# Kernel optimization log

Measured on AMD Instinct MI355X. Metric: run time of the kernel, lower is better.

Reference implementation:

```python
import jax, jax.numpy as jnp
import numpy as np

LEAKY = 0.2  # tf.nn.leaky_relu default alpha
E_SZ = [64, 64, 16]
F_SZ = [128, 128, 8]
N_MAPS, C, H, W = 64, 1, 32, 32
B = 8192


def _leaky(x):
    return jnp.where(x >= 0, x, LEAKY * x)


def func_theta(x, theta, sz, in_sz):
    # x: [B, in_sz]; theta: [B, total]; per-sample MLP with weights sliced from theta
    y = x
    offset = 0
    n = len(sz)
    for i, out_sz in enumerate(sz):
        w_sz = in_sz * out_sz
        Wm = theta[:, offset:offset + w_sz].reshape(-1, in_sz, out_sz)
        offset += w_sz
        b = theta[:, offset:offset + out_sz]
        offset += out_sz
        y = jnp.einsum('bi,bio->bo', y, Wm) + b
        if i < n - 1:
            y = _leaky(y)
        in_sz = out_sz
    return y


def setup_inputs() -> dict:
    key = jax.random.key(0)
    ks = jax.random.split(key, 16)

    def g(k, shape, scale):
        return (jax.random.normal(k, shape, dtype=jnp.float32) * scale)

    inp = {
        'indices': jax.random.randint(ks[0], (B,), 0, N_MAPS, dtype=jnp.int32),
        'states': jax.random.normal(ks[1], (B, 4), dtype=jnp.float32),
        'maps': jax.random.normal(ks[2], (N_MAPS, C, H, W), dtype=jnp.float32),
        'fc1_w': g(ks[3], (C * H * W, 256), 1.0 / np.sqrt(C * H * W)),
        'fc1_b': jnp.zeros((256,), jnp.float32),
        'fc2_w': g(ks[4], (256, 128), 1.0 / np.sqrt(256)),
        'fc2_b': jnp.zeros((128,), jnp.float32),
        'fc3_w': g(ks[5], (128, 128), 1.0 / np.sqrt(128)),
        'fc3_b': jnp.zeros((128,), jnp.float32),
        'bn_w': g(ks[6], (128, 32), 1.0 / np.sqrt(128)),
        'bn_b': jnp.zeros((32,), jnp.float32),
        'e_w': g(ks[7], (32, 5456), 1e-5),
        'e_b': g(ks[8], (5456,), 1e-3),
        'f_w': g(ks[9], (32, 21768), 1e-5),
        'f_b': g(ks[10], (21768,), 1e-3),
    }
    return inp


def reference(indices, states, maps, fc1_w, fc1_b, fc2_w, fc2_b, fc3_w, fc3_b,
              bn_w, bn_b, e_w, e_b, f_w, f_b):
    # gather maps per sample and flatten (NCHW -> NHWC transpose is a no-op after flatten
    # mathematically, but keep the exact data layout of the original)
    m = jnp.transpose(maps[indices], (0, 2, 3, 1)).astype(jnp.float32)  # [B,H,W,C]
    z = m.reshape(m.shape[0], -1)

    # hypernet trunk
    z = _leaky(z @ fc1_w + fc1_b)
    z = _leaky(z @ fc2_w + fc2_b)
    z = _leaky(z @ fc3_w + fc3_b)
    z = z @ bn_w + bn_b  # bottleneck, no activation
    theta_e = z @ e_w + e_b  # [B, 5456]
    theta_f = z @ f_w + f_b  # [B, 21768]

    S = states[:, 0:2]
    G = states[:, 2:4]
    e_s = func_theta(S, theta_e, E_SZ, 2)
    e_g = func_theta(G, theta_e, E_SZ, 2)
    zf = jnp.concatenate([e_s, e_g], axis=-1)  # [B, 32]
    ang = func_theta(zf, theta_f, F_SZ, 2 * E_SZ[-1])  # [B, 8]
    pts = jnp.concatenate([jnp.sin(ang), jnp.cos(ang)], axis=-1)  # [B, 16]
    return pts
```

## Files before the change

### kernel.cpp

```cpp
#include <hip/hip_runtime.h>
#include <hip/hip_bf16.h>


#define LEAKY 0.2f
#define NCLS 64
#define B_TOT 8192
#define NSLICE 4


__device__ __forceinline__ float lrelu(float x) { return x >= 0.f ? x : LEAKY * x; }

__global__ __launch_bounds__(1024) void backbone_bucket_kernel(
    const float* __restrict__ maps,
    const float* __restrict__ fc1_w, const float* __restrict__ fc1_b,
    const float* __restrict__ fc2_w, const float* __restrict__ fc2_b,
    const float* __restrict__ fc3_w, const float* __restrict__ fc3_b,
    const float* __restrict__ bn_w,  const float* __restrict__ bn_b,
    float* __restrict__ z,
    const int* __restrict__ idx, int* __restrict__ counts,
    int* __restrict__ offsets, int* __restrict__ perm)
{
    __shared__ float m[1024];
    __shared__ float red[1024];
    __shared__ float h1[256];
    __shared__ float h2[128];
    __shared__ float h3[128];
    __shared__ int cnt[16][64];
    __shared__ int wcur[16][64];

    const int t = threadIdx.x;

    if (blockIdx.x == 64) {
        const int w = t >> 6;
        cnt[w][t & 63] = 0;
        __syncthreads();
        int my[8];
#pragma unroll
        for (int r = 0; r < 8; ++r) {
            my[r] = idx[r * 1024 + t];
            atomicAdd(&cnt[w][my[r]], 1);
        }
        __syncthreads();
        if (t < 64) {
            int run = 0;
#pragma unroll
            for (int w2 = 0; w2 < 16; ++w2) {
                const int v = cnt[w2][t];
                wcur[w2][t] = run;
                run += v;
            }
            counts[t] = run;
            int x = run;
            for (int d = 1; d < 64; d <<= 1) {
                const int y = __shfl_up(x, d, 64);
                if (t >= d) x += y;
            }
            const int basec = x - run;
            offsets[t] = basec;
#pragma unroll
            for (int w2 = 0; w2 < 16; ++w2) wcur[w2][t] += basec;
        }
        __syncthreads();
#pragma unroll
        for (int r = 0; r < 8; ++r) {
            const int p = atomicAdd(&wcur[w][my[r]], 1);
            perm[p] = r * 1024 + t;
        }
        return;
    }

    const int c = blockIdx.x;
    m[t] = maps[(size_t)c * 1024 + t];
    __syncthreads();

    {
        const int o = t & 255, ks = t >> 8;
        const float* wp = fc1_w + o;
        float acc = 0.f;
#pragma unroll 8
        for (int i = 0; i < 256; ++i) {
            const int k = ks * 256 + i;
            acc += m[k] * wp[(size_t)k * 256];
        }
        red[t] = acc;
    }
    __syncthreads();
    if (t < 256)
        h1[t] = lrelu(fc1_b[t] + red[t] + red[256 + t] + red[512 + t] + red[768 + t]);
    __syncthreads();
    {
        const int o = t & 127, ks = t >> 7;
        float acc = 0.f;
#pragma unroll
        for (int i = 0; i < 32; ++i) {
            const int k = ks * 32 + i;
            acc += h1[k] * fc2_w[k * 128 + o];
        }
        red[t] = acc;
    }
    __syncthreads();
    if (t < 128) {
        float a = fc2_b[t];
#pragma unroll
        for (int r = 0; r < 8; ++r) a += red[r * 128 + t];
        h2[t] = lrelu(a);
    }
    __syncthreads();
    {
        const int o = t & 127, ks = t >> 7;
        float acc = 0.f;
#pragma unroll
        for (int i = 0; i < 16; ++i) {
            const int k = ks * 16 + i;
            acc += h2[k] * fc3_w[k * 128 + o];
        }
        red[t] = acc;
    }
    __syncthreads();
    if (t < 128) {
        float a = fc3_b[t];
#pragma unroll
        for (int r = 0; r < 8; ++r) a += red[r * 128 + t];
        h3[t] = lrelu(a);
    }
    __syncthreads();
    {
        const int o = t & 31, ks = t >> 5;
        float acc = 0.f;
#pragma unroll
        for (int i = 0; i < 4; ++i) {
            const int k = ks * 4 + i;
            acc += h3[k] * bn_w[k * 32 + o];
        }
        red[t] = acc;
    }
    __syncthreads();
    if (t < 32) {
        float a = bn_b[t];
#pragma unroll
        for (int r = 0; r < 32; ++r) a += red[r * 32 + t];
        z[c * 32 + t] = a;
    }
}

__global__ __launch_bounds__(256) void theta_kernel(
    const float* __restrict__ z,
    const float* __restrict__ e_w, const float* __restrict__ e_b,
    const float* __restrict__ f_w, const float* __restrict__ f_b,
    float* __restrict__ th_e, float* __restrict__ th_f)
{
    __shared__ __align__(16) float zl[2048];
    const int t = threadIdx.x;
    ((float4*)zl)[t]       = ((const float4*)z)[t];
    ((float4*)zl)[t + 256] = ((const float4*)z)[t + 256];
    __syncthreads();

    int j = blockIdx.x * 256 + t;
    const int cbase = blockIdx.y * 8;
    const float* wbase;
    float* op;
    int stride;
    float bias;
    if (j < 5456) {
        wbase = e_w + j; bias = e_b[j]; op = th_e + j; stride = 5456;
    } else {
        const int jj = j - 5456;
        if (jj >= 21768) return;
        wbase = f_w + jj; bias = f_b[jj]; op = th_f + jj; stride = 21768;
    }
    float wk[32];
#pragma unroll
    for (int k = 0; k < 32; ++k) wk[k] = wbase[(size_t)k * stride];

#pragma unroll
    for (int cc = 0; cc < 8; cc += 4) {
        const int c0 = cbase + cc;
        float a0 = bias, a1 = bias, a2 = bias, a3 = bias;
#pragma unroll
        for (int k4 = 0; k4 < 8; ++k4) {
            const float4 z0 = *(const float4*)&zl[(c0 + 0) * 32 + k4 * 4];
            const float4 z1 = *(const float4*)&zl[(c0 + 1) * 32 + k4 * 4];
            const float4 z2 = *(const float4*)&zl[(c0 + 2) * 32 + k4 * 4];
            const float4 z3 = *(const float4*)&zl[(c0 + 3) * 32 + k4 * 4];
            const float w0 = wk[k4 * 4], w1 = wk[k4 * 4 + 1];
            const float w2 = wk[k4 * 4 + 2], w3 = wk[k4 * 4 + 3];
            a0 += z0.x * w0 + z0.y * w1 + z0.z * w2 + z0.w * w3;
            a1 += z1.x * w0 + z1.y * w1 + z1.z * w2 + z1.w * w3;
            a2 += z2.x * w0 + z2.y * w1 + z2.z * w2 + z2.w * w3;
            a3 += z3.x * w0 + z3.y * w1 + z3.z * w2 + z3.w * w3;
        }
        op[(size_t)(c0 + 0) * stride] = a0;
        op[(size_t)(c0 + 1) * stride] = a1;
        op[(size_t)(c0 + 2) * stride] = a2;
        op[(size_t)(c0 + 3) * stride] = a3;
    }
}

#define ESTRIDE 68
#define FSTRIDE 132

__global__ __launch_bounds__(512) void func_kernel(
    const float* __restrict__ states,
    const float* __restrict__ th_e_all, const float* __restrict__ th_f_all,
    const int* __restrict__ counts, const int* __restrict__ offsets,
    const int* __restrict__ perm, float* __restrict__ out)
{
    __shared__ __align__(16) float wbuf[5392];
    __shared__ __align__(16) float w3fb[1160];
    __shared__ __align__(16) float actA[4352];
    __shared__ __align__(16) float actB[4352];

    const int c = blockIdx.x;
    const int s = blockIdx.y;
    const int nb   = counts[c];
    const int base = offsets[c];
    const int chunk = (nb + NSLICE - 1) / NSLICE;
    const int k0 = s * chunk;
    const int k1 = (nb < k0 + chunk) ? nb : (k0 + chunk);
    const int cnt = (k1 > k0) ? (k1 - k0) : 0;
    if (cnt == 0) return;

    const float* te = th_e_all + (size_t)c * 5456;
    const float* tf = th_f_all + (size_t)c * 21768;

    const int t  = threadIdx.x;
    const int b  = t & 31;
    const int ve = (t >> 5) & 1;
    const int vb = t & 63;
    const int ge = t >> 6;
    const int gf = t >> 5;
    const int cole = ge * 8;
    const int colf = gf * 8;
    const int eoff = vb * ESTRIDE;
    const int foff = b * FSTRIDE;

    for (int j = t * 4; j < 1160; j += 2048)
        *(float4*)&w3fb[j] = *(const float4*)&tf[20608 + j];
    for (int j = t * 4; j < 5392; j += 2048)
        *(float4*)&wbuf[j] = *(const float4*)&te[j];

    const int passes = (cnt + 31) >> 5;
    for (int p = 0; p < passes; ++p) {
        __syncthreads();
        if (p) {
            for (int j = t * 4; j < 5392; j += 2048)
                *(float4*)&wbuf[j] = *(const float4*)&te[j];
            __syncthreads();
        }

        const int kk = k0 + p * 32 + b;
        const bool valid = kk < k1;
        const int bi = valid ? perm[base + kk] : 0;
        const float2 sv = *(const float2*)&states[(size_t)bi * 4 + 2 * ve];

        {
            const float4 wa0 = *(const float4*)&wbuf[cole];
            const float4 wa1 = *(const float4*)&wbuf[cole + 4];
            const float4 wb0 = *(const float4*)&wbuf[64 + cole];
            const float4 wb1 = *(const float4*)&wbuf[64 + cole + 4];
            const float4 bb0 = *(const float4*)&wbuf[128 + cole];
            const float4 bb1 = *(const float4*)&wbuf[128 + cole + 4];
            float4 o0, o1;
            o0.x = lrelu(sv.x * wa0.x + sv.y * wb0.x + bb0.x);
            o0.y = lrelu(sv.x * wa0.y + sv.y * wb0.y + bb0.y);
            o0.z = lrelu(sv.x * wa0.z + sv.y * wb0.z + bb0.z);
            o0.w = lrelu(sv.x * wa0.w + sv.y * wb0.w + bb0.w);
            o1.x = lrelu(sv.x * wa1.x + sv.y * wb1.x + bb1.x);
            o1.y = lrelu(sv.x * wa1.y + sv.y * wb1.y + bb1.y);
            o1.z = lrelu(sv.x * wa1.z + sv.y * wb1.z + bb1.z);
            o1.w = lrelu(sv.x * wa1.w + sv.y * wb1.w + bb1.w);
            *(float4*)&actA[eoff + cole]     = o0;
            *(float4*)&actA[eoff + cole + 4] = o1;
        }
        __syncthreads();

        {
            float acc[8] = {0, 0, 0, 0, 0, 0, 0, 0};
#pragma unroll 4
            for (int i4 = 0; i4 < 16; ++i4) {
                const float4 y4 = *(const float4*)&actA[eoff + i4 * 4];
#pragma unroll
                for (int u = 0; u < 4; ++u) {
                    const int row = 192 + (i4 * 4 + u) * 64 + cole;
                    const float4 wA = *(const float4*)&wbuf[row];
                    const float4 wB = *(const float4*)&wbuf[row + 4];
                    const float yv = (&y4.x)[u];
                    acc[0] += yv * wA.x; acc[1] += yv * wA.y;
                    acc[2] += yv * wA.z; acc[3] += yv * wA.w;
                    acc[4] += yv * wB.x; acc[5] += yv * wB.y;
                    acc[6] += yv * wB.z; acc[7] += yv * wB.w;
                }
            }
            const float4 bA = *(const float4*)&wbuf[4288 + cole];
            const float4 bB = *(const float4*)&wbuf[4288 + cole + 4];
            float4 o0, o1;
            o0.x = lrelu(acc[0] + bA.x); o0.y = lrelu(acc[1] + bA.y);
            o0.z = lrelu(acc[2] + bA.z); o0.w = lrelu(acc[3] + bA.w);
            o1.x = lrelu(acc[4] + bB.x); o1.y = lrelu(acc[5] + bB.y);
            o1.z = lrelu(acc[6] + bB.z); o1.w = lrelu(acc[7] + bB.w);
            *(float4*)&actB[eoff + cole]     = o0;
            *(float4*)&actB[eoff + cole + 4] = o1;
        }
        __syncthreads();

        {
            const int col3 = ge * 2;
            float a0 = 0.f, a1 = 0.f;
#pragma unroll 4
            for (int i4 = 0; i4 < 16; ++i4) {
                const float4 y4 = *(const float4*)&actB[eoff + i4 * 4];
#pragma unroll
                for (int u = 0; u < 4; ++u) {
                    const int i = i4 * 4 + u;
                    const float yv = (&y4.x)[u];
                    a0 += yv * wbuf[4352 + i * 16 + col3];
                    a1 += yv * wbuf[4352 + i * 16 + col3 + 1];
                }
            }
            a0 += wbuf[5376 + col3];
            a1 += wbuf[5376 + col3 + 1];
            actA[foff + ve * 16 + col3]     = a0;
            actA[foff + ve * 16 + col3 + 1] = a1;
        }
        __syncthreads();

        for (int j = t * 4; j < 4224; j += 2048)
            *(float4*)&wbuf[j] = *(const float4*)&tf[j];
        __syncthreads();

        {
            float acc[8] = {0, 0, 0, 0, 0, 0, 0, 0};
#pragma unroll
            for (int i4 = 0; i4 < 8; ++i4) {
                const float4 y4 = *(const float4*)&actA[foff + i4 * 4];
#pragma unroll
                for (int u = 0; u < 4; ++u) {
                    const int row = (i4 * 4 + u) * 128 + colf;
                    const float4 wA = *(const float4*)&wbuf[row];
                    const float4 wB = *(const float4*)&wbuf[row + 4];
                    const float yv = (&y4.x)[u];
                    acc[0] += yv * wA.x; acc[1] += yv * wA.y;
                    acc[2] += yv * wA.z; acc[3] += yv * wA.w;
                    acc[4] += yv * wB.x; acc[5] += yv * wB.y;
                    acc[6] += yv * wB.z; acc[7] += yv * wB.w;
                }
            }
            const float4 bA = *(const float4*)&wbuf[4096 + colf];
            const float4 bB = *(const float4*)&wbuf[4096 + colf + 4];
            float4 o0, o1;
            o0.x = lrelu(acc[0] + bA.x); o0.y = lrelu(acc[1] + bA.y);
            o0.z = lrelu(acc[2] + bA.z); o0.w = lrelu(acc[3] + bA.w);
            o1.x = lrelu(acc[4] + bB.x); o1.y = lrelu(acc[5] + bB.y);
            o1.z = lrelu(acc[6] + bB.z); o1.w = lrelu(acc[7] + bB.w);
            *(float4*)&actB[foff + colf]     = o0;
            *(float4*)&actB[foff + colf + 4] = o1;
        }
        __syncthreads();

        {
            float acc[8] = {0, 0, 0, 0, 0, 0, 0, 0};
#pragma unroll
            for (int h = 0; h < 4; ++h) {
                if (h) __syncthreads();
                for (int j = t * 4; j < 4096; j += 2048)
                    *(float4*)&wbuf[j] = *(const float4*)&tf[4224 + h * 4096 + j];
                __syncthreads();
#pragma unroll 4
                for (int i4 = 0; i4 < 8; ++i4) {
                    const float4 y4 = *(const float4*)&actB[foff + h * 32 + i4 * 4];
#pragma unroll
                    for (int u = 0; u < 4; ++u) {
                        const int row = (i4 * 4 + u) * 128 + colf;
                        const float4 wA = *(const float4*)&wbuf[row];
                        const float4 wB = *(const float4*)&wbuf[row + 4];
                        const float yv = (&y4.x)[u];
                        acc[0] += yv * wA.x; acc[1] += yv * wA.y;
                        acc[2] += yv * wA.z; acc[3] += yv * wA.w;
                        acc[4] += yv * wB.x; acc[5] += yv * wB.y;
                        acc[6] += yv * wB.z; acc[7] += yv * wB.w;
                    }
                }
            }
            const float4 bA = *(const float4*)&w3fb[colf];
            const float4 bB = *(const float4*)&w3fb[colf + 4];
            float4 o0, o1;
            o0.x = lrelu(acc[0] + bA.x); o0.y = lrelu(acc[1] + bA.y);
            o0.z = lrelu(acc[2] + bA.z); o0.w = lrelu(acc[3] + bA.w);
            o1.x = lrelu(acc[4] + bB.x); o1.y = lrelu(acc[5] + bB.y);
            o1.z = lrelu(acc[6] + bB.z); o1.w = lrelu(acc[7] + bB.w);
            *(float4*)&actA[foff + colf]     = o0;
            *(float4*)&actA[foff + colf + 4] = o1;
        }
        __syncthreads();

        if (gf < 8) {
            float a = 0.f;
#pragma unroll 8
            for (int i4 = 0; i4 < 32; ++i4) {
                const float4 y4 = *(const float4*)&actA[foff + i4 * 4];
#pragma unroll
                for (int u = 0; u < 4; ++u)
                    a += (&y4.x)[u] * w3fb[128 + (i4 * 4 + u) * 8 + gf];
            }
            a += w3fb[1152 + gf];
            if (valid) {
                out[(size_t)bi * 16 + gf]     = __sinf(a);
                out[(size_t)bi * 16 + 8 + gf] = __cosf(a);
            }
        }
    }
}

extern "C" void kernel_launch(void* const* d_in, const int* in_sizes, int n_in,
                              void* d_out, int out_size, void* d_ws, size_t ws_size,
                              hipStream_t stream)
{
    const int*   indices = (const int*)  d_in[0];
    const float* states  = (const float*)d_in[1];
    const float* maps    = (const float*)d_in[2];
    const float* fc1_w   = (const float*)d_in[3];
    const float* fc1_b   = (const float*)d_in[4];
    const float* fc2_w   = (const float*)d_in[5];
    const float* fc2_b   = (const float*)d_in[6];
    const float* fc3_w   = (const float*)d_in[7];
    const float* fc3_b   = (const float*)d_in[8];
    const float* bn_w    = (const float*)d_in[9];
    const float* bn_b    = (const float*)d_in[10];
    const float* e_w     = (const float*)d_in[11];
    const float* e_b     = (const float*)d_in[12];
    const float* f_w     = (const float*)d_in[13];
    const float* f_b     = (const float*)d_in[14];
    float* out = (float*)d_out;

    float* ws   = (float*)d_ws;
    float* z    = ws;
    float* th_e = ws + 2048;
    float* th_f = ws + 351232;
    int* counts  = (int*)(ws + 1744384);
    int* offsets = counts + 64;
    int* perm    = counts + 128;

    backbone_bucket_kernel<<<65, 1024, 0, stream>>>(
        maps, fc1_w, fc1_b, fc2_w, fc2_b, fc3_w, fc3_b, bn_w, bn_b, z,
        indices, counts, offsets, perm);
    theta_kernel<<<dim3(107, 8), 256, 0, stream>>>(
        z, e_w, e_b, f_w, f_b, th_e, th_f);
    func_kernel<<<dim3(NCLS, NSLICE), 512, 0, stream>>>(
        states, th_e, th_f, counts, offsets, perm, out);
}
```

Measured before the change: 142.0 us.

## Keep full per-class theta weights resident in LDS across passes

The func kernel now loads the whole per-class theta_e and theta_f (about 140 KB) into dynamic LDS once, instead of reloading weight chunks from global memory on every 32-sample pass with extra barriers. Samples are assigned to slices round-robin in 32-sample blocks instead of contiguous chunks. This removes repeated global reloads and many __syncthreads. The cost is very high LDS usage, which limits each CU to one block, plus a larger upfront load before compute starts.

```diff
diff --git a/kernel.cpp b/kernel.cpp
--- a/kernel.cpp
+++ b/kernel.cpp
@@ -199,26 +199,28 @@
 #define ESTRIDE 68
 #define FSTRIDE 132
 
+#define K3_LDS_FLOATS 35864
+#define K3_LDS_BYTES  (K3_LDS_FLOATS * 4)
+
 __global__ __launch_bounds__(512) void func_kernel(
     const float* __restrict__ states,
     const float* __restrict__ th_e_all, const float* __restrict__ th_f_all,
     const int* __restrict__ counts, const int* __restrict__ offsets,
     const int* __restrict__ perm, float* __restrict__ out)
 {
-    __shared__ __align__(16) float wbuf[5392];
-    __shared__ __align__(16) float w3fb[1160];
-    __shared__ __align__(16) float actA[4352];
-    __shared__ __align__(16) float actB[4352];
+    extern __shared__ float smem[];
+    float* wE   = smem;
+    float* wF   = smem + 5392;
+    float* actA = smem + 27160;
+    float* actB = smem + 31512;
 
     const int c = blockIdx.x;
     const int s = blockIdx.y;
     const int nb   = counts[c];
     const int base = offsets[c];
-    const int chunk = (nb + NSLICE - 1) / NSLICE;
-    const int k0 = s * chunk;
-    const int k1 = (nb < k0 + chunk) ? nb : (k0 + chunk);
-    const int cnt = (k1 > k0) ? (k1 - k0) : 0;
-    if (cnt == 0) return;
+    const int nblk = (nb + 31) >> 5;
+    const int npass = (nblk > s) ? ((nblk - 1 - s) / NSLICE + 1) : 0;
+    if (npass == 0) return;
 
     const float* te = th_e_all + (size_t)c * 5456;
     const float* tf = th_f_all + (size_t)c * 21768;
@@ -234,32 +236,26 @@
     const int eoff = vb * ESTRIDE;
     const int foff = b * FSTRIDE;
 
-    for (int j = t * 4; j < 1160; j += 2048)
-        *(float4*)&w3fb[j] = *(const float4*)&tf[20608 + j];
     for (int j = t * 4; j < 5392; j += 2048)
-        *(float4*)&wbuf[j] = *(const float4*)&te[j];
-
-    const int passes = (cnt + 31) >> 5;
-    for (int p = 0; p < passes; ++p) {
-        __syncthreads();
-        if (p) {
-            for (int j = t * 4; j < 5392; j += 2048)
-                *(float4*)&wbuf[j] = *(const float4*)&te[j];
-            __syncthreads();
-        }
-
-        const int kk = k0 + p * 32 + b;
-        const bool valid = kk < k1;
+        *(float4*)&wE[j] = *(const float4*)&te[j];
+    for (int j = t * 4; j < 21768; j += 2048)
+        *(float4*)&wF[j] = *(const float4*)&tf[j];
+
+    for (int p = 0; p < npass; ++p) {
+        __syncthreads();
+
+        const int kk = ((p * NSLICE + s) << 5) + b;
+        const bool valid = kk < nb;
         const int bi = valid ? perm[base + kk] : 0;
         const float2 sv = *(const float2*)&states[(size_t)bi * 4 + 2 * ve];
 
         {
-            const float4 wa0 = *(const float4*)&wbuf[cole];
-            const float4 wa1 = *(const float4*)&wbuf[cole + 4];
-            const float4 wb0 = *(const float4*)&wbuf[64 + cole];
-            const float4 wb1 = *(const float4*)&wbuf[64 + cole + 4];
-            const float4 bb0 = *(const float4*)&wbuf[128 + cole];
-            const float4 bb1 = *(const float4*)&wbuf[128 + cole + 4];
+            const float4 wa0 = *(const float4*)&wE[cole];
+            const float4 wa1 = *(const float4*)&wE[cole + 4];
+            const float4 wb0 = *(const float4*)&wE[64 + cole];
+            const float4 wb1 = *(const float4*)&wE[64 + cole + 4];
+            const float4 bb0 = *(const float4*)&wE[128 + cole];
+            const float4 bb1 = *(const float4*)&wE[128 + cole + 4];
             float4 o0, o1;
             o0.x = lrelu(sv.x * wa0.x + sv.y * wb0.x + bb0.x);
             o0.y = lrelu(sv.x * wa0.y + sv.y * wb0.y + bb0.y);
@@ -282,8 +278,8 @@
 #pragma unroll
                 for (int u = 0; u < 4; ++u) {
                     const int row = 192 + (i4 * 4 + u) * 64 + cole;
-                    const float4 wA = *(const float4*)&wbuf[row];
-                    const float4 wB = *(const float4*)&wbuf[row + 4];
+                    const float4 wA = *(const float4*)&wE[row];
+                    const float4 wB = *(const float4*)&wE[row + 4];
                     const float yv = (&y4.x)[u];
                     acc[0] += yv * wA.x; acc[1] += yv * wA.y;
                     acc[2] += yv * wA.z; acc[3] += yv * wA.w;
@@ -291,8 +287,8 @@
                     acc[6] += yv * wB.z; acc[7] += yv * wB.w;
                 }
             }
-            const float4 bA = *(const float4*)&wbuf[4288 + cole];
-            const float4 bB = *(const float4*)&wbuf[4288 + cole + 4];
+            const float4 bA = *(const float4*)&wE[4288 + cole];
+            const float4 bB = *(const float4*)&wE[4288 + cole + 4];
             float4 o0, o1;
             o0.x = lrelu(acc[0] + bA.x); o0.y = lrelu(acc[1] + bA.y);
             o0.z = lrelu(acc[2] + bA.z); o0.w = lrelu(acc[3] + bA.w);
@@ -313,21 +309,18 @@
                 for (int u = 0; u < 4; ++u) {
                     const int i = i4 * 4 + u;
                     const float yv = (&y4.x)[u];
-                    a0 += yv * wbuf[4352 + i * 16 + col3];
-                    a1 += yv * wbuf[4352 + i * 16 + col3 + 1];
+                    const float2 w2 = *(const float2*)&wE[4352 + i * 16 + col3];
+                    a0 += yv * w2.x;
+                    a1 += yv * w2.y;
                 }
             }
-            a0 += wbuf[5376 + col3];
-            a1 += wbuf[5376 + col3 + 1];
+            a0 += wE[5376 + col3];
+            a1 += wE[5376 + col3 + 1];
             actA[foff + ve * 16 + col3]     = a0;
             actA[foff + ve * 16 + col3 + 1] = a1;
         }
         __syncthreads();
 
-        for (int j = t * 4; j < 4224; j += 2048)
-            *(float4*)&wbuf[j] = *(const float4*)&tf[j];
-        __syncthreads();
-
         {
             float acc[8] = {0, 0, 0, 0, 0, 0, 0, 0};
 #pragma unroll
@@ -336,8 +329,8 @@
 #pragma unroll
                 for (int u = 0; u < 4; ++u) {
                     const int row = (i4 * 4 + u) * 128 + colf;
-                    const float4 wA = *(const float4*)&wbuf[row];
-                    const float4 wB = *(const float4*)&wbuf[row + 4];
+                    const float4 wA = *(const float4*)&wF[row];
+                    const float4 wB = *(const float4*)&wF[row + 4];
                     const float yv = (&y4.x)[u];
                     acc[0] += yv * wA.x; acc[1] += yv * wA.y;
                     acc[2] += yv * wA.z; acc[3] += yv * wA.w;
@@ -345,8 +338,8 @@
                     acc[6] += yv * wB.z; acc[7] += yv * wB.w;
                 }
             }
-            const float4 bA = *(const float4*)&wbuf[4096 + colf];
-            const float4 bB = *(const float4*)&wbuf[4096 + colf + 4];
+            const float4 bA = *(const float4*)&wF[4096 + colf];
+            const float4 bB = *(const float4*)&wF[4096 + colf + 4];
             float4 o0, o1;
             o0.x = lrelu(acc[0] + bA.x); o0.y = lrelu(acc[1] + bA.y);
             o0.z = lrelu(acc[2] + bA.z); o0.w = lrelu(acc[3] + bA.w);
@@ -359,30 +352,23 @@
 
         {
             float acc[8] = {0, 0, 0, 0, 0, 0, 0, 0};
-#pragma unroll
-            for (int h = 0; h < 4; ++h) {
-                if (h) __syncthreads();
-                for (int j = t * 4; j < 4096; j += 2048)
-                    *(float4*)&wbuf[j] = *(const float4*)&tf[4224 + h * 4096 + j];
-                __syncthreads();
 #pragma unroll 4
-                for (int i4 = 0; i4 < 8; ++i4) {
-                    const float4 y4 = *(const float4*)&actB[foff + h * 32 + i4 * 4];
-#pragma unroll
-                    for (int u = 0; u < 4; ++u) {
-                        const int row = (i4 * 4 + u) * 128 + colf;
-                        const float4 wA = *(const float4*)&wbuf[row];
-                        const float4 wB = *(const float4*)&wbuf[row + 4];
-                        const float yv = (&y4.x)[u];
-                        acc[0] += yv * wA.x; acc[1] += yv * wA.y;
-                        acc[2] += yv * wA.z; acc[3] += yv * wA.w;
-                        acc[4] += yv * wB.x; acc[5] += yv * wB.y;
-                        acc[6] += yv * wB.z; acc[7] += yv * wB.w;
-                    }
+            for (int i4 = 0; i4 < 32; ++i4) {
+                const float4 y4 = *(const float4*)&actB[foff + i4 * 4];
+#pragma unroll
+                for (int u = 0; u < 4; ++u) {
+                    const int row = 4224 + (i4 * 4 + u) * 128 + colf;
+                    const float4 wA = *(const float4*)&wF[row];
+                    const float4 wB = *(const float4*)&wF[row + 4];
+                    const float yv = (&y4.x)[u];
+                    acc[0] += yv * wA.x; acc[1] += yv * wA.y;
+                    acc[2] += yv * wA.z; acc[3] += yv * wA.w;
+                    acc[4] += yv * wB.x; acc[5] += yv * wB.y;
+                    acc[6] += yv * wB.z; acc[7] += yv * wB.w;
                 }
             }
-            const float4 bA = *(const float4*)&w3fb[colf];
-            const float4 bB = *(const float4*)&w3fb[colf + 4];
+            const float4 bA = *(const float4*)&wF[20608 + colf];
+            const float4 bB = *(const float4*)&wF[20608 + colf + 4];
             float4 o0, o1;
             o0.x = lrelu(acc[0] + bA.x); o0.y = lrelu(acc[1] + bA.y);
             o0.z = lrelu(acc[2] + bA.z); o0.w = lrelu(acc[3] + bA.w);
@@ -400,9 +386,9 @@
                 const float4 y4 = *(const float4*)&actA[foff + i4 * 4];
 #pragma unroll
                 for (int u = 0; u < 4; ++u)
-                    a += (&y4.x)[u] * w3fb[128 + (i4 * 4 + u) * 8 + gf];
-            }
-            a += w3fb[1152 + gf];
+                    a += (&y4.x)[u] * wF[20736 + (i4 * 4 + u) * 8 + gf];
+            }
+            a += wF[21760 + gf];
             if (valid) {
                 out[(size_t)bi * 16 + gf]     = __sinf(a);
                 out[(size_t)bi * 16 + 8 + gf] = __cosf(a);
@@ -440,11 +426,19 @@
     int* offsets = counts + 64;
     int* perm    = counts + 128;
 
+    static int s_lds_optin = 0;
+    if (!s_lds_optin) {
+        hipFuncSetAttribute((const void*)func_kernel,
+                            hipFuncAttributeMaxDynamicSharedMemorySize,
+                            K3_LDS_BYTES);
+        s_lds_optin = 1;
+    }
+
     backbone_bucket_kernel<<<65, 1024, 0, stream>>>(
         maps, fc1_w, fc1_b, fc2_w, fc2_b, fc3_w, fc3_b, bn_w, bn_b, z,
         indices, counts, offsets, perm);
     theta_kernel<<<dim3(107, 8), 256, 0, stream>>>(
         z, e_w, e_b, f_w, f_b, th_e, th_f);
-    func_kernel<<<dim3(NCLS, NSLICE), 512, 0, stream>>>(
+    func_kernel<<<dim3(NCLS, NSLICE), 512, K3_LDS_BYTES, stream>>>(
         states, th_e, th_f, counts, offsets, perm, out);
 }
```

Result: no change. 139.7 us (-1.6%).
